# Performance work log

Measured on AMD Instinct MI355X. Metric: run time of the kernel, lower is better.

Reference implementation:

```python
import jax, jax.numpy as jnp
import numpy as np
from jax import lax

B, C, H, W = 2, 96, 96, 96
N = 8            # d_state
R = C // 16      # dt_rank = 6
K = 4            # scan directions


def _gn(x, g, b, eps=1e-5):
    # GroupNorm(num_groups=1): normalize over (C,H,W) per sample, per-channel affine
    mu = jnp.mean(x, axis=(1, 2, 3), keepdims=True)
    var = jnp.var(x, axis=(1, 2, 3), keepdims=True)
    xn = (x - mu) * jax.lax.rsqrt(var + eps)
    return xn * g[None, :, None, None] + b[None, :, None, None]


def _conv1x1(x, w, b):
    return jnp.einsum('bchw,oc->bohw', x, w) + b[None, :, None, None]


def _ss2d(x, xproj_w, dt_w, dt_b, A_log, Ds):
    # x: [B,C,H,W]. 4-directional selective scan (VMamba SS2D core).
    Bn, Cc, Hh, Ww = x.shape
    L = Hh * Ww
    x_hw = x.reshape(Bn, Cc, L)                                   # row-major
    x_wh = jnp.transpose(x, (0, 1, 3, 2)).reshape(Bn, Cc, L)      # col-major
    xs = jnp.stack([x_hw, x_wh, x_hw[..., ::-1], x_wh[..., ::-1]], axis=1)  # [B,K,C,L]
    xdbl = jnp.einsum('bkcl,kdc->bkdl', xs, xproj_w)              # [B,K,R+2N,L]
    dts, Bs, Cs = jnp.split(xdbl, [R, R + N], axis=2)             # [B,K,R,L],[B,K,N,L],[B,K,N,L]
    dts = jax.nn.softplus(jnp.einsum('bkrl,kcr->bkcl', dts, dt_w) + dt_b[None, :, :, None])  # [B,K,C,L]
    A = -jnp.exp(A_log)                                           # [K,C,N]
    dA = jnp.exp(dts[:, :, :, None, :] * A[None, :, :, :, None])                    # [B,K,C,N,L]
    dBx = dts[:, :, :, None, :] * Bs[:, :, None, :, :] * xs[:, :, :, None, :]       # [B,K,C,N,L]

    def comb(e1, e2):
        a1, b1 = e1
        a2, b2 = e2
        return a1 * a2, a2 * b1 + b2

    _, hs = lax.associative_scan(comb, (dA, dBx), axis=-1)        # h_t = dA_t*h_{t-1} + dBx_t
    ys = jnp.einsum('bkcnl,bknl->bkcl', hs, Cs) + Ds[None, :, :, None] * xs
    y0 = ys[:, 0]
    y1 = jnp.transpose(ys[:, 1].reshape(Bn, Cc, Ww, Hh), (0, 1, 3, 2)).reshape(Bn, Cc, L)
    y2 = ys[:, 2][..., ::-1]
    y3 = jnp.transpose(ys[:, 3][..., ::-1].reshape(Bn, Cc, Ww, Hh), (0, 1, 3, 2)).reshape(Bn, Cc, L)
    return (y0 + y1 + y2 + y3).reshape(Bn, Cc, Hh, Ww)


def setup_inputs() -> dict:
    key = jax.random.key(0)
    ks = jax.random.split(key, 12)
    f = lambda k, sh: jax.random.normal(k, sh, jnp.float32) * 0.02
    return {
        'x': jax.random.normal(ks[0], (B, C, H, W), jnp.float32),
        'ln_g': jnp.ones((C,), jnp.float32), 'ln_b': jnp.zeros((C,), jnp.float32),
        'p1_w': f(ks[1], (C, C)), 'p1_b': jnp.zeros((C,), jnp.float32),
        'p2_w': f(ks[2], (C, C)), 'p2_b': jnp.zeros((C,), jnp.float32),
        'dw_w': f(ks[3], (C, 1, 3, 3)), 'dw_b': jnp.zeros((C,), jnp.float32),
        'xproj_w': f(ks[4], (K, R + 2 * N, C)),
        'dt_w': f(ks[5], (K, C, R)), 'dt_b': f(ks[6], (K, C)),
        'A_log': jnp.log(jnp.broadcast_to(jnp.arange(1, N + 1, dtype=jnp.float32), (K, C, N))),
        'Ds': jnp.ones((K, C), jnp.float32),
        'n2_g': jnp.ones((C,), jnp.float32), 'n2_b': jnp.zeros((C,), jnp.float32),
        'ca_w1': f(ks[7], (C // 8, C)), 'ca_b1': jnp.zeros((C // 8,), jnp.float32),
        'ca_w2': f(ks[8], (C, C // 8)), 'ca_b2': jnp.zeros((C,), jnp.float32),
    }


def reference(x, ln_g, ln_b, p1_w, p1_b, p2_w, p2_b, dw_w, dw_b,
              xproj_w, dt_w, dt_b, A_log, Ds, n2_g, n2_b,
              ca_w1, ca_b1, ca_w2, ca_b2):
    h = _gn(x, ln_g, ln_b)
    a = jax.nn.silu(_conv1x1(h, p1_w, p1_b))                       # path 1
    b = _conv1x1(h, p2_w, p2_b)                                    # path 2
    b = lax.conv_general_dilated(b, dw_w, (1, 1), ((1, 1), (1, 1)),
                                 feature_group_count=C,
                                 dimension_numbers=('NCHW', 'OIHW', 'NCHW'))
    b = b + dw_b[None, :, None, None]
    b = jax.nn.silu(b)
    b = _ss2d(b, xproj_w, dt_w, dt_b, A_log, Ds)
    b = _gn(b, n2_g, n2_b)
    y = a * b
    # channel attention (SE-style, reduction 8)
    s = jnp.mean(y, axis=(2, 3))                                   # [B,C]
    z = jax.nn.relu(s @ ca_w1.T + ca_b1)
    attn = jax.nn.sigmoid(z @ ca_w2.T + ca_b2)
    y = y * attn[:, :, None, None]
    return x + y
```

## Files before the change

### kernel.cpp

```cpp
#include <hip/hip_runtime.h>
#include <hip/hip_bf16.h>
#include <cmath>
#include <cstdint>

constexpr int B_ = 2, C_ = 96, H_ = 96, W_ = 96, L_ = H_ * W_;
constexpr int N_ = 8, R_ = 6, K_ = 4, D_ = R_ + 2 * N_;
constexpr int CH_ = 128, G_ = L_ / CH_;
constexpr int JS_ = 4, SEG_ = CH_ / JS_;
constexpr int S_ = G_ * JS_;
constexpr float EPS_ = 1e-5f;

__device__ __forceinline__ float silu_f(float v) { return v / (1.f + __expf(-v)); }
__device__ __forceinline__ float softplus_f(float t) {
    return fmaxf(t, 0.f) + __logf(1.f + __expf(-fabsf(t)));
}

__device__ __forceinline__ void block_reduce2(float& a, float& b) {
    #pragma unroll
    for (int o = 32; o; o >>= 1) { a += __shfl_xor(a, o); b += __shfl_xor(b, o); }
    __shared__ float la[4], lb[4];
    int wid = threadIdx.x >> 6;
    if ((threadIdx.x & 63) == 0) { la[wid] = a; lb[wid] = b; }
    __syncthreads();
    if (threadIdx.x == 0) { a = la[0] + la[1] + la[2] + la[3]; b = lb[0] + lb[1] + lb[2] + lb[3]; }
}

__global__ __launch_bounds__(256) void stats_kernel(const float* __restrict__ in,
                                                    float* __restrict__ stats, int outbase) {
    int b = blockIdx.y;
    const float* p = in + (size_t)b * ((size_t)C_ * L_);
    float s = 0.f, s2 = 0.f;
    const int total = C_ * L_;
    for (int i = blockIdx.x * 256 + threadIdx.x; i < total; i += gridDim.x * 256) {
        float v = p[i];
        s += v;
        s2 = fmaf(v, v, s2);
    }
    block_reduce2(s, s2);
    if (threadIdx.x == 0) {
        atomicAdd(&stats[outbase + 2 * b], s);
        atomicAdd(&stats[outbase + 2 * b + 1], s2);
    }
}

__global__ __launch_bounds__(256) void conv1x1_kernel(
    const float* __restrict__ x, const float* __restrict__ stats,
    const float* __restrict__ lng, const float* __restrict__ lnb,
    const float* __restrict__ w1, const float* __restrict__ b1,
    const float* __restrict__ w2, const float* __restrict__ b2,
    float* __restrict__ a, float* __restrict__ bpre) {
    constexpr int OG = 8;
    int b = blockIdx.z;
    int o0 = blockIdx.y * OG;
    int l = blockIdx.x * 256 + threadIdx.x;

    constexpr float inv = 1.f / (float)(C_ * L_);
    float mu = stats[2 * b] * inv;
    float var = stats[2 * b + 1] * inv - mu * mu;
    float rs = rsqrtf(var + EPS_);

    __shared__ float sw1[OG][C_], sw2[OG][C_], sg[C_], so[C_];
    for (int i = threadIdx.x; i < OG * C_; i += 256) {
        int j = i / C_, c = i % C_;
        sw1[j][c] = w1[(o0 + j) * C_ + c];
        sw2[j][c] = w2[(o0 + j) * C_ + c];
    }
    for (int i = threadIdx.x; i < C_; i += 256) {
        float g = lng[i];
        sg[i] = g * rs;
        so[i] = lnb[i] - mu * rs * g;
    }
    __syncthreads();

    const float* xb = x + (size_t)b * C_ * L_ + l;
    float acc1[OG], acc2[OG];
    #pragma unroll
    for (int j = 0; j < OG; ++j) { acc1[j] = b1[o0 + j]; acc2[j] = b2[o0 + j]; }
    for (int c = 0; c < C_; ++c) {
        float hv = fmaf(xb[(size_t)c * L_], sg[c], so[c]);
        #pragma unroll
        for (int j = 0; j < OG; ++j) {
            acc1[j] = fmaf(hv, sw1[j][c], acc1[j]);
            acc2[j] = fmaf(hv, sw2[j][c], acc2[j]);
        }
    }
    #pragma unroll
    for (int j = 0; j < OG; ++j) {
        size_t o = ((size_t)(b * C_ + o0 + j)) * L_ + l;
        a[o] = silu_f(acc1[j]);
        bpre[o] = acc2[j];
    }
}

__global__ __launch_bounds__(256) void dw_kernel(const float* __restrict__ bp,
                                                 const float* __restrict__ wgt,
                                                 const float* __restrict__ bias,
                                                 float* __restrict__ u) {
    int b = blockIdx.z, c = blockIdx.y;
    int pix = blockIdx.x * 256 + threadIdx.x;
    int h = pix / W_, w = pix % W_;
    const float* in = bp + ((size_t)(b * C_ + c)) * L_;
    const float* kw = wgt + c * 9;
    float acc = bias[c];
    #pragma unroll
    for (int dh = -1; dh <= 1; ++dh) {
        int hh = h + dh;
        if (hh < 0 || hh >= H_) continue;
        #pragma unroll
        for (int dw = -1; dw <= 1; ++dw) {
            int ww = w + dw;
            if (ww < 0 || ww >= W_) continue;
            acc = fmaf(in[hh * W_ + ww], kw[(dh + 1) * 3 + (dw + 1)], acc);
        }
    }
    u[((size_t)(b * C_ + c)) * L_ + pix] = silu_f(acc);
}

__global__ __launch_bounds__(256) void transpose_kernel(const float* __restrict__ u,
                                                        float* __restrict__ u_t) {
    int w0 = blockIdx.x * 32;
    int c = blockIdx.y, b = blockIdx.z;
    __shared__ float ts[96][33];
    const float* src = u + ((size_t)(b * C_ + c)) * L_;
    float* dst = u_t + ((size_t)(b * C_ + c)) * L_;
    for (int idx = threadIdx.x; idx < 96 * 32; idx += 256) {
        int hh = idx >> 5, ww = idx & 31;
        ts[hh][ww] = src[hh * 96 + w0 + ww];
    }
    __syncthreads();
    for (int idx = threadIdx.x; idx < 32 * 96; idx += 256) {
        int ww = idx / 96, hh = idx % 96;
        dst[(w0 + ww) * 96 + hh] = ts[hh][ww];
    }
}

__global__ __launch_bounds__(256) void proj_kernel(
    const float* __restrict__ u, const float* __restrict__ u_t,
    const float* __restrict__ xproj,
    float* __restrict__ dts, float* __restrict__ Bsb, float* __restrict__ Csb) {
    int b = blockIdx.z, k = blockIdx.y;
    int pos = threadIdx.x & 63, cg = threadIdx.x >> 6;
    int l = blockIdx.x * 64 + pos;

    __shared__ float sxp[C_][24];
    __shared__ float red[D_][4][64];
    for (int i = threadIdx.x; i < D_ * C_; i += 256) {
        int d = i / C_, c = i % C_;
        sxp[c][d] = xproj[(k * D_ + d) * C_ + c];
    }
    __syncthreads();

    const float* src = ((k & 1) ? u_t : u) + (size_t)b * C_ * L_;
    int posIdx = (k < 2) ? l : (L_ - 1 - l);
    const float* sp = src + (size_t)(cg * 24) * L_ + posIdx;

    float acc[D_];
    #pragma unroll
    for (int d = 0; d < D_; ++d) acc[d] = 0.f;
    #pragma unroll 4
    for (int ci = 0; ci < 24; ++ci) {
        int c = cg * 24 + ci;
        float xv = sp[(size_t)ci * L_];
        float w[22];
        *(float4*)&w[0]  = *(const float4*)&sxp[c][0];
        *(float4*)&w[4]  = *(const float4*)&sxp[c][4];
        *(float4*)&w[8]  = *(const float4*)&sxp[c][8];
        *(float4*)&w[12] = *(const float4*)&sxp[c][12];
        *(float4*)&w[16] = *(const float4*)&sxp[c][16];
        *(float2*)&w[20] = *(const float2*)&sxp[c][20];
        #pragma unroll
        for (int d = 0; d < D_; ++d) acc[d] = fmaf(xv, w[d], acc[d]);
    }
    #pragma unroll
    for (int d = 0; d < D_; ++d) red[d][cg][pos] = acc[d];
    __syncthreads();

    if (cg == 0) {
        #pragma unroll
        for (int r = 0; r < R_; ++r) {
            float s = red[r][0][pos] + red[r][1][pos] + red[r][2][pos] + red[r][3][pos];
            dts[((size_t)((b * K_ + k) * R_ + r)) * L_ + l] = s;
        }
    } else if (cg == 1) {
        #pragma unroll
        for (int n = 0; n < N_; ++n) {
            int d = R_ + n;
            float s = red[d][0][pos] + red[d][1][pos] + red[d][2][pos] + red[d][3][pos];
            Bsb[((size_t)((b * K_ + k) * N_ + n)) * L_ + l] = s;
        }
    } else if (cg == 2) {
        #pragma unroll
        for (int n = 0; n < N_; ++n) {
            int d = R_ + N_ + n;
            float s = red[d][0][pos] + red[d][1][pos] + red[d][2][pos] + red[d][3][pos];
            Csb[((size_t)((b * K_ + k) * N_ + n)) * L_ + l] = s;
        }
    }
}


__global__ __launch_bounds__(192) void scan1_kernel(
    const float* __restrict__ dts, const float* __restrict__ dtw,
    const float* __restrict__ dtbv, const float* __restrict__ Bs,
    const float* __restrict__ u, const float* __restrict__ u_t,
    const float* __restrict__ A_log,
    float* __restrict__ carA, float* __restrict__ carB) {
    int g = blockIdx.x >> 1, chalf = blockIdx.x & 1;
    int k = blockIdx.y, b = blockIdx.z;
    int c0 = chalf * 48;
    const int t = threadIdx.x;
    const int l0 = g * CH_;

    __shared__ float u_s[48][132];
    __shared__ float B_s[128][12];
    __shared__ float T_s[128][8];

    const float* usrc = ((k & 1) ? u_t : u) + (size_t)b * C_ * L_ + (size_t)c0 * L_;
    if (k < 2) {
        for (int idx = t; idx < 48 * 32; idx += 192) {
            int c2 = idx >> 5, q = idx & 31;
            *(float4*)&u_s[c2][q * 4] = *(const float4*)(usrc + (size_t)c2 * L_ + l0 + q * 4);
        }
    } else {
        for (int idx = t; idx < 48 * 32; idx += 192) {
            int c2 = idx >> 5, q = idx & 31;
            float4 v = *(const float4*)(usrc + (size_t)c2 * L_ + (L_ - l0 - q * 4 - 4));
            u_s[c2][q * 4 + 0] = v.w; u_s[c2][q * 4 + 1] = v.z;
            u_s[c2][q * 4 + 2] = v.y; u_s[c2][q * 4 + 3] = v.x;
        }
    }
    const float* Bg = Bs + ((size_t)(b * K_ + k)) * N_ * L_ + l0;
    for (int idx = t; idx < 8 * 32; idx += 192) {
        int n = idx >> 5, q = idx & 31;
        float4 v = *(const float4*)(Bg + (size_t)n * L_ + q * 4);
        B_s[q * 4 + 0][n] = v.x; B_s[q * 4 + 1][n] = v.y;
        B_s[q * 4 + 2][n] = v.z; B_s[q * 4 + 3][n] = v.w;
    }
    const float* Tg = dts + ((size_t)(b * K_ + k)) * R_ * L_ + l0;
    for (int idx = t; idx < 6 * 32; idx += 192) {
        int r = idx >> 5, q = idx & 31;
        float4 v = *(const float4*)(Tg + (size_t)r * L_ + q * 4);
        T_s[q * 4 + 0][r] = v.x; T_s[q * 4 + 1][r] = v.y;
        T_s[q * 4 + 2][r] = v.z; T_s[q * 4 + 3][r] = v.w;
    }
    __syncthreads();

    int cc = t % 48, j = t / 48;
    int c = c0 + cc;
    float A[N_];
    #pragma unroll
    for (int n = 0; n < N_; ++n) A[n] = -__expf(A_log[(k * C_ + c) * N_ + n]);
    float wdt[R_];
    #pragma unroll
    for (int r = 0; r < R_; ++r) wdt[r] = dtw[(k * C_ + c) * R_ + r];
    float bdt = dtbv[k * C_ + c];

    float ap[N_], h[N_];
    #pragma unroll
    for (int n = 0; n < N_; ++n) { ap[n] = 1.f; h[n] = 0.f; }
    int i0 = j * SEG_;
    for (int ii = 0; ii < SEG_; ii += 4) {
        float4 x4 = *(float4*)&u_s[cc][i0 + ii];
        float xx[4] = {x4.x, x4.y, x4.z, x4.w};
        #pragma unroll
        for (int s = 0; s < 4; ++s) {
            int i = i0 + ii + s;
            float4 t4 = *(float4*)&T_s[i][0];
            float2 t2 = *(float2*)&T_s[i][4];
            float tt = bdt;
            tt = fmaf(t4.x, wdt[0], tt); tt = fmaf(t4.y, wdt[1], tt);
            tt = fmaf(t4.z, wdt[2], tt); tt = fmaf(t4.w, wdt[3], tt);
            tt = fmaf(t2.x, wdt[4], tt); tt = fmaf(t2.y, wdt[5], tt);
            float d = softplus_f(tt);
            float dx = d * xx[s];
            float4 ba = *(float4*)&B_s[i][0];
            float4 bb = *(float4*)&B_s[i][4];
            float bv[8] = {ba.x, ba.y, ba.z, ba.w, bb.x, bb.y, bb.z, bb.w};
            #pragma unroll
            for (int n = 0; n < N_; ++n) {
                float da = __expf(d * A[n]);
                ap[n] *= da;
                h[n] = fmaf(da, h[n], bv[n] * dx);
            }
        }
    }
    size_t sidx = (((size_t)((b * K_ + k) * C_ + c)) * S_ + (g * JS_ + j)) * N_;
    #pragma unroll
    for (int n = 0; n < N_; ++n) { carA[sidx + n] = ap[n]; carB[sidx + n] = h[n]; }
}

__global__ __launch_bounds__(256) void scan2_kernel(const float* __restrict__ carA,
                                                    const float* __restrict__ carB,
                                                    float* __restrict__ hinit) {
    int tid = blockIdx.x * 256 + threadIdx.x;
    if (tid >= B_ * K_ * C_ * N_) return;
    int n = tid & 7;
    size_t rowb = (size_t)(tid >> 3) * S_;
    float h = 0.f;
    for (int s = 0; s < S_; s += 8) {
        float av[8], bv[8];
        #pragma unroll
        for (int q = 0; q < 8; ++q) {
            size_t idx = (rowb + s + q) * N_ + n;
            av[q] = carA[idx]; bv[q] = carB[idx];
        }
        #pragma unroll
        for (int q = 0; q < 8; ++q) {
            size_t idx = (rowb + s + q) * N_ + n;
            hinit[idx] = h;
            h = fmaf(av[q], h, bv[q]);
        }
    }
}

__global__ __launch_bounds__(192) void scan3_kernel(
    const float* __restrict__ dts, const float* __restrict__ dtw,
    const float* __restrict__ dtbv, const float* __restrict__ Bs,
    const float* __restrict__ Cs, const float* __restrict__ u,
    const float* __restrict__ u_t, const float* __restrict__ A_log,
    const float* __restrict__ Dsv, const float* __restrict__ hinit,
    float* __restrict__ ydir) {
    int g = blockIdx.x >> 1, chalf = blockIdx.x & 1;
    int k = blockIdx.y, b = blockIdx.z;
    int c0 = chalf * 48;
    const int t = threadIdx.x;
    const int l0 = g * CH_;

    __shared__ float u_s[48][132];
    __shared__ float B_s[128][12];
    __shared__ float C_s[128][12];
    __shared__ float T_s[128][8];

    const float* usrc = ((k & 1) ? u_t : u) + (size_t)b * C_ * L_ + (size_t)c0 * L_;
    if (k < 2) {
        for (int idx = t; idx < 48 * 32; idx += 192) {
            int c2 = idx >> 5, q = idx & 31;
            *(float4*)&u_s[c2][q * 4] = *(const float4*)(usrc + (size_t)c2 * L_ + l0 + q * 4);
        }
    } else {
        for (int idx = t; idx < 48 * 32; idx += 192) {
            int c2 = idx >> 5, q = idx & 31;
            float4 v = *(const float4*)(usrc + (size_t)c2 * L_ + (L_ - l0 - q * 4 - 4));
            u_s[c2][q * 4 + 0] = v.w; u_s[c2][q * 4 + 1] = v.z;
            u_s[c2][q * 4 + 2] = v.y; u_s[c2][q * 4 + 3] = v.x;
        }
    }
    const float* Bg = Bs + ((size_t)(b * K_ + k)) * N_ * L_ + l0;
    const float* Cg = Cs + ((size_t)(b * K_ + k)) * N_ * L_ + l0;
    for (int idx = t; idx < 8 * 32; idx += 192) {
        int n = idx >> 5, q = idx & 31;
        float4 v = *(const float4*)(Bg + (size_t)n * L_ + q * 4);
        B_s[q * 4 + 0][n] = v.x; B_s[q * 4 + 1][n] = v.y;
        B_s[q * 4 + 2][n] = v.z; B_s[q * 4 + 3][n] = v.w;
        float4 w = *(const float4*)(Cg + (size_t)n * L_ + q * 4);
        C_s[q * 4 + 0][n] = w.x; C_s[q * 4 + 1][n] = w.y;
        C_s[q * 4 + 2][n] = w.z; C_s[q * 4 + 3][n] = w.w;
    }
    const float* Tg = dts + ((size_t)(b * K_ + k)) * R_ * L_ + l0;
    for (int idx = t; idx < 6 * 32; idx += 192) {
        int r = idx >> 5, q = idx & 31;
        float4 v = *(const float4*)(Tg + (size_t)r * L_ + q * 4);
        T_s[q * 4 + 0][r] = v.x; T_s[q * 4 + 1][r] = v.y;
        T_s[q * 4 + 2][r] = v.z; T_s[q * 4 + 3][r] = v.w;
    }
    __syncthreads();

    int cc = t % 48, j = t / 48;
    int c = c0 + cc;
    float A[N_];
    #pragma unroll
    for (int n = 0; n < N_; ++n) A[n] = -__expf(A_log[(k * C_ + c) * N_ + n]);
    float wdt[R_];
    #pragma unroll
    for (int r = 0; r < R_; ++r) wdt[r] = dtw[(k * C_ + c) * R_ + r];
    float bdt = dtbv[k * C_ + c];
    float Dv = Dsv[k * C_ + c];

    float h[N_];
    size_t sidx = (((size_t)((b * K_ + k) * C_ + c)) * S_ + (g * JS_ + j)) * N_;
    #pragma unroll
    for (int n = 0; n < N_; ++n) h[n] = hinit[sidx + n];

    int i0 = j * SEG_;
    for (int ii = 0; ii < SEG_; ii += 4) {
        float4 x4 = *(float4*)&u_s[cc][i0 + ii];
        float xx[4] = {x4.x, x4.y, x4.z, x4.w};
        #pragma unroll
        for (int s = 0; s < 4; ++s) {
            int i = i0 + ii + s;
            float4 t4 = *(float4*)&T_s[i][0];
            float2 t2 = *(float2*)&T_s[i][4];
            float tt = bdt;
            tt = fmaf(t4.x, wdt[0], tt); tt = fmaf(t4.y, wdt[1], tt);
            tt = fmaf(t4.z, wdt[2], tt); tt = fmaf(t4.w, wdt[3], tt);
            tt = fmaf(t2.x, wdt[4], tt); tt = fmaf(t2.y, wdt[5], tt);
            float d = softplus_f(tt);
            float dx = d * xx[s];
            float4 ba = *(float4*)&B_s[i][0];
            float4 bb = *(float4*)&B_s[i][4];
            float4 ca = *(float4*)&C_s[i][0];
            float4 cb = *(float4*)&C_s[i][4];
            float bv[8] = {ba.x, ba.y, ba.z, ba.w, bb.x, bb.y, bb.z, bb.w};
            float cv[8] = {ca.x, ca.y, ca.z, ca.w, cb.x, cb.y, cb.z, cb.w};
            float y = Dv * xx[s];
            #pragma unroll
            for (int n = 0; n < N_; ++n) {
                float da = __expf(d * A[n]);
                h[n] = fmaf(da, h[n], bv[n] * dx);
                y = fmaf(cv[n], h[n], y);
            }
            u_s[cc][i] = y;
        }
    }
    __syncthreads();
    float* yg = ydir + ((size_t)((b * K_ + k) * C_ + c0)) * L_ + l0;
    for (int idx = t; idx < 48 * 32; idx += 192) {
        int c2 = idx >> 5, q = idx & 31;
        *(float4*)(yg + (size_t)c2 * L_ + q * 4) = *(float4*)&u_s[c2][q * 4];
    }
}

__global__ __launch_bounds__(256) void merge_kernel(const float* __restrict__ ydir,
                                                    float* __restrict__ ysum,
                                                    float* __restrict__ stats) {
    int h0 = blockIdx.x * 32;
    int c = blockIdx.y, b = blockIdx.z;
    __shared__ float t1[96][33], t3[96][33];
    const float* y0p = ydir + ((size_t)((b * K_ + 0) * C_ + c)) * L_;
    const float* y1p = ydir + ((size_t)((b * K_ + 1) * C_ + c)) * L_;
    const float* y2p = ydir + ((size_t)((b * K_ + 2) * C_ + c)) * L_;
    const float* y3p = ydir + ((size_t)((b * K_ + 3) * C_ + c)) * L_;
    for (int idx = threadIdx.x; idx < 96 * 32; idx += 256) {
        int w = idx >> 5, hh = idx & 31;
        t1[w][hh] = y1p[w * 96 + h0 + hh];
        t3[w][hh] = y3p[L_ - 1 - (w * 96 + h0 + hh)];
    }
    __syncthreads();
    float s = 0.f, s2 = 0.f;
    float* yout = ysum + ((size_t)(b * C_ + c)) * L_;
    for (int idx = threadIdx.x; idx < 32 * 96; idx += 256) {
        int hh = idx / 96, w = idx % 96;
        int pix = (h0 + hh) * 96 + w;
        float v = y0p[pix] + y2p[L_ - 1 - pix] + t1[w][hh] + t3[w][hh];
        yout[pix] = v;
        s += v;
        s2 = fmaf(v, v, s2);
    }
    block_reduce2(s, s2);
    if (threadIdx.x == 0) {
        atomicAdd(&stats[4 + 2 * b], s);
        atomicAdd(&stats[5 + 2 * b], s2);
    }
}

__global__ __launch_bounds__(256) void gn2_kernel(
    const float* __restrict__ ysum, const float* __restrict__ a,
    const float* __restrict__ stats, const float* __restrict__ g2,
    const float* __restrict__ b2, float* __restrict__ yv, float* __restrict__ svec) {
    int b = blockIdx.z, c = blockIdx.y;
    int pix = blockIdx.x * 256 + threadIdx.x;
    constexpr float inv = 1.f / (float)(C_ * L_);
    float mu = stats[4 + 2 * b] * inv;
    float var = stats[5 + 2 * b] * inv - mu * mu;
    float rs = rsqrtf(var + EPS_);
    size_t o = ((size_t)(b * C_ + c)) * L_ + pix;
    float bn = fmaf((ysum[o] - mu) * rs, g2[c], b2[c]);
    float y = a[o] * bn;
    yv[o] = y;

    float s = y;
    #pragma unroll
    for (int off = 32; off; off >>= 1) s += __shfl_xor(s, off);
    __shared__ float ls[4];
    if ((threadIdx.x & 63) == 0) ls[threadIdx.x >> 6] = s;
    __syncthreads();
    if (threadIdx.x == 0) atomicAdd(&svec[b * C_ + c], ls[0] + ls[1] + ls[2] + ls[3]);
}

__global__ __launch_bounds__(128) void attn_kernel(
    const float* __restrict__ svec, const float* __restrict__ w1,
    const float* __restrict__ b1, const float* __restrict__ w2,
    const float* __restrict__ b2, float* __restrict__ attn) {
    int b = blockIdx.x;
    __shared__ float ss[C_];
    __shared__ float zz[C_ / 8];
    int t = threadIdx.x;
    if (t < C_) ss[t] = svec[b * C_ + t] * (1.f / (float)L_);
    __syncthreads();
    if (t < C_ / 8) {
        float acc = b1[t];
        for (int c = 0; c < C_; ++c) acc = fmaf(w1[t * C_ + c], ss[c], acc);
        zz[t] = fmaxf(acc, 0.f);
    }
    __syncthreads();
    if (t < C_) {
        float acc = b2[t];
        #pragma unroll
        for (int j = 0; j < C_ / 8; ++j) acc = fmaf(w2[t * (C_ / 8) + j], zz[j], acc);
        attn[b * C_ + t] = 1.f / (1.f + __expf(-acc));
    }
}

__global__ __launch_bounds__(256) void final_kernel(const float* __restrict__ x,
                                                    const float* __restrict__ yv,
                                                    const float* __restrict__ attn,
                                                    float* __restrict__ out) {
    int b = blockIdx.z, c = blockIdx.y;
    int pix = blockIdx.x * 256 + threadIdx.x;
    size_t o = ((size_t)(b * C_ + c)) * L_ + pix;
    out[o] = fmaf(yv[o], attn[b * C_ + c], x[o]);
}

extern "C" void kernel_launch(void* const* d_in, const int* in_sizes, int n_in,
                              void* d_out, int out_size, void* d_ws, size_t ws_size,
                              hipStream_t stream) {
    const float* x    = (const float*)d_in[0];
    const float* ln_g = (const float*)d_in[1];
    const float* ln_b = (const float*)d_in[2];
    const float* p1w  = (const float*)d_in[3];
    const float* p1b  = (const float*)d_in[4];
    const float* p2w  = (const float*)d_in[5];
    const float* p2b  = (const float*)d_in[6];
    const float* dww  = (const float*)d_in[7];
    const float* dwb  = (const float*)d_in[8];
    const float* xprj = (const float*)d_in[9];
    const float* dtw  = (const float*)d_in[10];
    const float* dtb  = (const float*)d_in[11];
    const float* Alog = (const float*)d_in[12];
    const float* Dsp  = (const float*)d_in[13];
    const float* n2g  = (const float*)d_in[14];
    const float* n2b  = (const float*)d_in[15];
    const float* caw1 = (const float*)d_in[16];
    const float* cab1 = (const float*)d_in[17];
    const float* caw2 = (const float*)d_in[18];
    const float* cab2 = (const float*)d_in[19];
    float* out = (float*)d_out;

    const size_t BCL = (size_t)B_ * C_ * L_ * sizeof(float);
    char* ws = (char*)d_ws;
    size_t off = 0;
    float* stats = (float*)(ws + off); off += 4096;
    float* a     = (float*)(ws + off); off += BCL;
    float* bpre  = (float*)(ws + off); off += BCL;
    float* u     = (float*)(ws + off); off += BCL;
    float* u_t   = (float*)(ws + off); off += BCL;
    float* dts   = (float*)(ws + off); off += (size_t)B_ * K_ * R_ * L_ * sizeof(float);
    float* Bsb   = (float*)(ws + off); off += (size_t)B_ * K_ * N_ * L_ * sizeof(float);
    float* Csb   = (float*)(ws + off); off += (size_t)B_ * K_ * N_ * L_ * sizeof(float);
    float* carB  = (float*)(ws + off); off += (size_t)B_ * K_ * C_ * S_ * N_ * sizeof(float);
    float* hinit = (float*)(ws + off); off += (size_t)B_ * K_ * C_ * S_ * N_ * sizeof(float);
    float* ydir  = (float*)(ws + off); off += (size_t)B_ * K_ * C_ * L_ * sizeof(float);
    float* carA = bpre;
    float* ysum = u;
    float* yv   = ydir;

    hipMemsetAsync(stats, 0, 4096, stream);

    stats_kernel<<<dim3(432, 2), 256, 0, stream>>>(x, stats, 0);
    conv1x1_kernel<<<dim3(36, 12, 2), 256, 0, stream>>>(x, stats, ln_g, ln_b,
                                                        p1w, p1b, p2w, p2b, a, bpre);
    dw_kernel<<<dim3(36, 96, 2), 256, 0, stream>>>(bpre, dww, dwb, u);
    transpose_kernel<<<dim3(3, 96, 2), 256, 0, stream>>>(u, u_t);
    proj_kernel<<<dim3(144, 4, 2), 256, 0, stream>>>(u, u_t, xprj, dts, Bsb, Csb);
    scan1_kernel<<<dim3(2 * G_, K_, B_), 192, 0, stream>>>(dts, dtw, dtb, Bsb, u, u_t,
                                                           Alog, carA, carB);
    scan2_kernel<<<24, 256, 0, stream>>>(carA, carB, hinit);
    scan3_kernel<<<dim3(2 * G_, K_, B_), 192, 0, stream>>>(dts, dtw, dtb, Bsb, Csb, u, u_t,
                                                           Alog, Dsp, hinit, ydir);
    merge_kernel<<<dim3(3, 96, 2), 256, 0, stream>>>(ydir, ysum, stats);
    gn2_kernel<<<dim3(36, 96, 2), 256, 0, stream>>>(ysum, a, stats, n2g, n2b, yv, stats + 16);
    attn_kernel<<<2, 128, 0, stream>>>(stats + 16, caw1, cab1, caw2, cab2, stats + 256);
    final_kernel<<<dim3(36, 96, 2), 256, 0, stream>>>(x, yv, stats + 256, out);
}
```

Measured before the change: 331.4 us.

## Fold GN into conv weights, fuse dwconv+transpose, and fold GN2 into SE statistics

A prep kernel pre-scales the 1x1 conv weights by the GroupNorm gain and precomputes per-output bias terms, so the conv loop becomes a plain FMA with the normalization applied once per output. The depthwise conv and the transpose are merged into one shared-memory stripe kernel that writes u and u_t together. The merge kernel also accumulates per-channel sums of a and a*ysum, so the SE mean is derived algebraically and the gn2 pass and the yv buffer are no longer needed. This removes two full-tensor passes and one launch, at the cost of a serial single-block prep kernel and a formula for the channel mean that is more sensitive to rounding.

```diff
diff --git a/kernel.cpp b/kernel.cpp
--- a/kernel.cpp
+++ b/kernel.cpp
@@ -25,8 +25,26 @@
     if (threadIdx.x == 0) { a = la[0] + la[1] + la[2] + la[3]; b = lb[0] + lb[1] + lb[2] + lb[3]; }
 }
 
+__device__ __forceinline__ void block_reduce4(float& a, float& b, float& c, float& d) {
+    #pragma unroll
+    for (int o = 32; o; o >>= 1) {
+        a += __shfl_xor(a, o); b += __shfl_xor(b, o);
+        c += __shfl_xor(c, o); d += __shfl_xor(d, o);
+    }
+    __shared__ float ls[4][4];
+    int wid = threadIdx.x >> 6;
+    if ((threadIdx.x & 63) == 0) { ls[wid][0] = a; ls[wid][1] = b; ls[wid][2] = c; ls[wid][3] = d; }
+    __syncthreads();
+    if (threadIdx.x == 0) {
+        a = ls[0][0] + ls[1][0] + ls[2][0] + ls[3][0];
+        b = ls[0][1] + ls[1][1] + ls[2][1] + ls[3][1];
+        c = ls[0][2] + ls[1][2] + ls[2][2] + ls[3][2];
+        d = ls[0][3] + ls[1][3] + ls[2][3] + ls[3][3];
+    }
+}
+
 __global__ __launch_bounds__(256) void stats_kernel(const float* __restrict__ in,
-                                                    float* __restrict__ stats, int outbase) {
+                                                    float* __restrict__ stats) {
     int b = blockIdx.y;
     const float* p = in + (size_t)b * ((size_t)C_ * L_);
     float s = 0.f, s2 = 0.f;
@@ -38,20 +56,39 @@
     }
     block_reduce2(s, s2);
     if (threadIdx.x == 0) {
-        atomicAdd(&stats[outbase + 2 * b], s);
-        atomicAdd(&stats[outbase + 2 * b + 1], s2);
-    }
+        atomicAdd(&stats[2 * b], s);
+        atomicAdd(&stats[2 * b + 1], s2);
+    }
+}
+
+__global__ __launch_bounds__(192) void prep_kernel(
+    const float* __restrict__ lng, const float* __restrict__ lnb,
+    const float* __restrict__ w1, const float* __restrict__ w2,
+    float* __restrict__ wmt, float* __restrict__ pq) {
+    int t = threadIdx.x;
+    int mat = t / 96, o = t % 96;
+    const float* w = (mat == 0 ? w1 : w2) + o * C_;
+    float* dst = wmt + ((size_t)(mat * 12 + o / 8) * C_) * 8 + (o % 8);
+    float P = 0.f, Q = 0.f;
+    for (int c = 0; c < C_; ++c) {
+        float wv = w[c];
+        float g = lng[c];
+        P = fmaf(lnb[c], wv, P);
+        Q = fmaf(g, wv, Q);
+        dst[c * 8] = g * wv;
+    }
+    pq[mat * 192 + o] = P;
+    pq[mat * 192 + 96 + o] = Q;
 }
 
 __global__ __launch_bounds__(256) void conv1x1_kernel(
     const float* __restrict__ x, const float* __restrict__ stats,
-    const float* __restrict__ lng, const float* __restrict__ lnb,
-    const float* __restrict__ w1, const float* __restrict__ b1,
-    const float* __restrict__ w2, const float* __restrict__ b2,
+    const float* __restrict__ wmt, const float* __restrict__ pq,
+    const float* __restrict__ b1, const float* __restrict__ b2,
     float* __restrict__ a, float* __restrict__ bpre) {
     constexpr int OG = 8;
-    int b = blockIdx.z;
-    int o0 = blockIdx.y * OG;
+    int b = blockIdx.z, by = blockIdx.y;
+    int o0 = by * OG;
     int l = blockIdx.x * 256 + threadIdx.x;
 
     constexpr float inv = 1.f / (float)(C_ * L_);
@@ -59,78 +96,90 @@
     float var = stats[2 * b + 1] * inv - mu * mu;
     float rs = rsqrtf(var + EPS_);
 
-    __shared__ float sw1[OG][C_], sw2[OG][C_], sg[C_], so[C_];
-    for (int i = threadIdx.x; i < OG * C_; i += 256) {
-        int j = i / C_, c = i % C_;
-        sw1[j][c] = w1[(o0 + j) * C_ + c];
-        sw2[j][c] = w2[(o0 + j) * C_ + c];
-    }
-    for (int i = threadIdx.x; i < C_; i += 256) {
-        float g = lng[i];
-        sg[i] = g * rs;
-        so[i] = lnb[i] - mu * rs * g;
+    __shared__ float s1[C_][OG], s2[C_][OG];
+    const float* w1p = wmt + ((size_t)(0 * 12 + by) * C_) * 8;
+    const float* w2p = wmt + ((size_t)(1 * 12 + by) * C_) * 8;
+    for (int i = threadIdx.x; i < C_ * OG / 4; i += 256) {
+        ((float4*)s1)[i] = ((const float4*)w1p)[i];
+        ((float4*)s2)[i] = ((const float4*)w2p)[i];
     }
     __syncthreads();
 
     const float* xb = x + (size_t)b * C_ * L_ + l;
     float acc1[OG], acc2[OG];
     #pragma unroll
-    for (int j = 0; j < OG; ++j) { acc1[j] = b1[o0 + j]; acc2[j] = b2[o0 + j]; }
+    for (int j = 0; j < OG; ++j) { acc1[j] = 0.f; acc2[j] = 0.f; }
     for (int c = 0; c < C_; ++c) {
-        float hv = fmaf(xb[(size_t)c * L_], sg[c], so[c]);
-        #pragma unroll
-        for (int j = 0; j < OG; ++j) {
-            acc1[j] = fmaf(hv, sw1[j][c], acc1[j]);
-            acc2[j] = fmaf(hv, sw2[j][c], acc2[j]);
-        }
-    }
+        float xv = xb[(size_t)c * L_];
+        float4 wa = *(const float4*)&s1[c][0];
+        float4 wb = *(const float4*)&s1[c][4];
+        float4 wc = *(const float4*)&s2[c][0];
+        float4 wd = *(const float4*)&s2[c][4];
+        acc1[0] = fmaf(xv, wa.x, acc1[0]); acc1[1] = fmaf(xv, wa.y, acc1[1]);
+        acc1[2] = fmaf(xv, wa.z, acc1[2]); acc1[3] = fmaf(xv, wa.w, acc1[3]);
+        acc1[4] = fmaf(xv, wb.x, acc1[4]); acc1[5] = fmaf(xv, wb.y, acc1[5]);
+        acc1[6] = fmaf(xv, wb.z, acc1[6]); acc1[7] = fmaf(xv, wb.w, acc1[7]);
+        acc2[0] = fmaf(xv, wc.x, acc2[0]); acc2[1] = fmaf(xv, wc.y, acc2[1]);
+        acc2[2] = fmaf(xv, wc.z, acc2[2]); acc2[3] = fmaf(xv, wc.w, acc2[3]);
+        acc2[4] = fmaf(xv, wd.x, acc2[4]); acc2[5] = fmaf(xv, wd.y, acc2[5]);
+        acc2[6] = fmaf(xv, wd.z, acc2[6]); acc2[7] = fmaf(xv, wd.w, acc2[7]);
+    }
+    float murs = mu * rs;
     #pragma unroll
     for (int j = 0; j < OG; ++j) {
-        size_t o = ((size_t)(b * C_ + o0 + j)) * L_ + l;
-        a[o] = silu_f(acc1[j]);
-        bpre[o] = acc2[j];
-    }
-}
-
-__global__ __launch_bounds__(256) void dw_kernel(const float* __restrict__ bp,
-                                                 const float* __restrict__ wgt,
-                                                 const float* __restrict__ bias,
-                                                 float* __restrict__ u) {
-    int b = blockIdx.z, c = blockIdx.y;
-    int pix = blockIdx.x * 256 + threadIdx.x;
-    int h = pix / W_, w = pix % W_;
+        int o = o0 + j;
+        size_t oo = ((size_t)(b * C_ + o)) * L_ + l;
+        float be1 = b1[o] + pq[o] - murs * pq[96 + o];
+        float be2 = b2[o] + pq[192 + o] - murs * pq[288 + o];
+        a[oo] = silu_f(fmaf(rs, acc1[j], be1));
+        bpre[oo] = fmaf(rs, acc2[j], be2);
+    }
+}
+
+__global__ __launch_bounds__(256) void dwt_kernel(const float* __restrict__ bp,
+                                                  const float* __restrict__ wgt,
+                                                  const float* __restrict__ bias,
+                                                  float* __restrict__ u,
+                                                  float* __restrict__ u_t) {
+    int stripe = blockIdx.x, c = blockIdx.y, b = blockIdx.z;
+    int h0 = stripe * 48;
+    __shared__ float in_s[50][96];
+    __shared__ float out_s[48][97];
     const float* in = bp + ((size_t)(b * C_ + c)) * L_;
+    for (int idx = threadIdx.x; idx < 50 * 96; idx += 256) {
+        int r = idx / 96, w = idx % 96;
+        int hh = h0 - 1 + r;
+        in_s[r][w] = (hh >= 0 && hh < 96) ? in[hh * 96 + w] : 0.f;
+    }
+    __syncthreads();
     const float* kw = wgt + c * 9;
-    float acc = bias[c];
-    #pragma unroll
-    for (int dh = -1; dh <= 1; ++dh) {
-        int hh = h + dh;
-        if (hh < 0 || hh >= H_) continue;
-        #pragma unroll
-        for (int dw = -1; dw <= 1; ++dw) {
-            int ww = w + dw;
-            if (ww < 0 || ww >= W_) continue;
-            acc = fmaf(in[hh * W_ + ww], kw[(dh + 1) * 3 + (dw + 1)], acc);
-        }
-    }
-    u[((size_t)(b * C_ + c)) * L_ + pix] = silu_f(acc);
-}
-
-__global__ __launch_bounds__(256) void transpose_kernel(const float* __restrict__ u,
-                                                        float* __restrict__ u_t) {
-    int w0 = blockIdx.x * 32;
-    int c = blockIdx.y, b = blockIdx.z;
-    __shared__ float ts[96][33];
-    const float* src = u + ((size_t)(b * C_ + c)) * L_;
-    float* dst = u_t + ((size_t)(b * C_ + c)) * L_;
-    for (int idx = threadIdx.x; idx < 96 * 32; idx += 256) {
-        int hh = idx >> 5, ww = idx & 31;
-        ts[hh][ww] = src[hh * 96 + w0 + ww];
-    }
-    __syncthreads();
-    for (int idx = threadIdx.x; idx < 32 * 96; idx += 256) {
-        int ww = idx / 96, hh = idx % 96;
-        dst[(w0 + ww) * 96 + hh] = ts[hh][ww];
+    float k0 = kw[0], k1 = kw[1], k2 = kw[2], k3 = kw[3], k4 = kw[4],
+          k5 = kw[5], k6 = kw[6], k7 = kw[7], k8 = kw[8];
+    float bs = bias[c];
+    float* up = u + ((size_t)(b * C_ + c)) * L_;
+    for (int idx = threadIdx.x; idx < 48 * 96; idx += 256) {
+        int r = idx / 96, w = idx % 96;
+        int ri = r + 1;
+        bool wl = (w > 0), wr = (w < 95);
+        float acc = bs;
+        acc = fmaf(wl ? in_s[ri - 1][w - 1] : 0.f, k0, acc);
+        acc = fmaf(in_s[ri - 1][w], k1, acc);
+        acc = fmaf(wr ? in_s[ri - 1][w + 1] : 0.f, k2, acc);
+        acc = fmaf(wl ? in_s[ri][w - 1] : 0.f, k3, acc);
+        acc = fmaf(in_s[ri][w], k4, acc);
+        acc = fmaf(wr ? in_s[ri][w + 1] : 0.f, k5, acc);
+        acc = fmaf(wl ? in_s[ri + 1][w - 1] : 0.f, k6, acc);
+        acc = fmaf(in_s[ri + 1][w], k7, acc);
+        acc = fmaf(wr ? in_s[ri + 1][w + 1] : 0.f, k8, acc);
+        float v = silu_f(acc);
+        up[(h0 + r) * 96 + w] = v;
+        out_s[r][w] = v;
+    }
+    __syncthreads();
+    float* tp = u_t + ((size_t)(b * C_ + c)) * L_;
+    for (int idx = threadIdx.x; idx < 96 * 48; idx += 256) {
+        int w = idx / 48, r = idx % 48;
+        tp[w * 96 + h0 + r] = out_s[r][w];
     }
 }
 
@@ -421,6 +470,7 @@
 }
 
 __global__ __launch_bounds__(256) void merge_kernel(const float* __restrict__ ydir,
+                                                    const float* __restrict__ a,
                                                     float* __restrict__ ysum,
                                                     float* __restrict__ stats) {
     int h0 = blockIdx.x * 32;
@@ -436,79 +486,81 @@
         t3[w][hh] = y3p[L_ - 1 - (w * 96 + h0 + hh)];
     }
     __syncthreads();
-    float s = 0.f, s2 = 0.f;
+    float s = 0.f, s2 = 0.f, m0 = 0.f, m1 = 0.f;
     float* yout = ysum + ((size_t)(b * C_ + c)) * L_;
+    const float* ap = a + ((size_t)(b * C_ + c)) * L_;
     for (int idx = threadIdx.x; idx < 32 * 96; idx += 256) {
         int hh = idx / 96, w = idx % 96;
         int pix = (h0 + hh) * 96 + w;
         float v = y0p[pix] + y2p[L_ - 1 - pix] + t1[w][hh] + t3[w][hh];
+        float av = ap[pix];
         yout[pix] = v;
         s += v;
         s2 = fmaf(v, v, s2);
-    }
-    block_reduce2(s, s2);
+        m0 += av;
+        m1 = fmaf(av, v, m1);
+    }
+    block_reduce4(s, s2, m0, m1);
     if (threadIdx.x == 0) {
         atomicAdd(&stats[4 + 2 * b], s);
         atomicAdd(&stats[5 + 2 * b], s2);
-    }
-}
-
-__global__ __launch_bounds__(256) void gn2_kernel(
-    const float* __restrict__ ysum, const float* __restrict__ a,
+        atomicAdd(&stats[16 + b * C_ + c], m0);
+        atomicAdd(&stats[256 + b * C_ + c], m1);
+    }
+}
+
+__global__ __launch_bounds__(128) void attn_kernel(
     const float* __restrict__ stats, const float* __restrict__ g2,
-    const float* __restrict__ b2, float* __restrict__ yv, float* __restrict__ svec) {
+    const float* __restrict__ b2, const float* __restrict__ w1,
+    const float* __restrict__ b1, const float* __restrict__ w2,
+    const float* __restrict__ b2a, float* __restrict__ attn) {
+    int b = blockIdx.x;
+    constexpr float inv = 1.f / (float)(C_ * L_);
+    float mu = stats[4 + 2 * b] * inv;
+    float var = stats[5 + 2 * b] * inv - mu * mu;
+    float rs = rsqrtf(var + EPS_);
+    __shared__ float ss[C_];
+    __shared__ float zz[12];
+    int t = threadIdx.x;
+    if (t < C_) {
+        float M0 = stats[16 + b * C_ + t];
+        float M1 = stats[256 + b * C_ + t];
+        ss[t] = (g2[t] * rs * (M1 - mu * M0) + b2[t] * M0) * (1.f / (float)L_);
+    }
+    __syncthreads();
+    if (t < 12) {
+        float acc = b1[t];
+        for (int c = 0; c < C_; ++c) acc = fmaf(w1[t * C_ + c], ss[c], acc);
+        zz[t] = fmaxf(acc, 0.f);
+    }
+    __syncthreads();
+    if (t < C_) {
+        float acc = b2a[t];
+        #pragma unroll
+        for (int j = 0; j < 12; ++j) acc = fmaf(w2[t * 12 + j], zz[j], acc);
+        attn[b * C_ + t] = 1.f / (1.f + __expf(-acc));
+    }
+}
+
+__global__ __launch_bounds__(256) void final_kernel(const float* __restrict__ x,
+                                                    const float* __restrict__ ysum,
+                                                    const float* __restrict__ a,
+                                                    const float* __restrict__ stats,
+                                                    const float* __restrict__ g2,
+                                                    const float* __restrict__ b2,
+                                                    const float* __restrict__ attn,
+                                                    float* __restrict__ out) {
     int b = blockIdx.z, c = blockIdx.y;
     int pix = blockIdx.x * 256 + threadIdx.x;
     constexpr float inv = 1.f / (float)(C_ * L_);
     float mu = stats[4 + 2 * b] * inv;
     float var = stats[5 + 2 * b] * inv - mu * mu;
     float rs = rsqrtf(var + EPS_);
+    float gc = g2[c] * rs, bc = b2[c] - mu * rs * g2[c];
+    float at = attn[b * C_ + c];
     size_t o = ((size_t)(b * C_ + c)) * L_ + pix;
-    float bn = fmaf((ysum[o] - mu) * rs, g2[c], b2[c]);
-    float y = a[o] * bn;
-    yv[o] = y;
-
-    float s = y;
-    #pragma unroll
-    for (int off = 32; off; off >>= 1) s += __shfl_xor(s, off);
-    __shared__ float ls[4];
-    if ((threadIdx.x & 63) == 0) ls[threadIdx.x >> 6] = s;
-    __syncthreads();
-    if (threadIdx.x == 0) atomicAdd(&svec[b * C_ + c], ls[0] + ls[1] + ls[2] + ls[3]);
-}
-
-__global__ __launch_bounds__(128) void attn_kernel(
-    const float* __restrict__ svec, const float* __restrict__ w1,
-    const float* __restrict__ b1, const float* __restrict__ w2,
-    const float* __restrict__ b2, float* __restrict__ attn) {
-    int b = blockIdx.x;
-    __shared__ float ss[C_];
-    __shared__ float zz[C_ / 8];
-    int t = threadIdx.x;
-    if (t < C_) ss[t] = svec[b * C_ + t] * (1.f / (float)L_);
-    __syncthreads();
-    if (t < C_ / 8) {
-        float acc = b1[t];
-        for (int c = 0; c < C_; ++c) acc = fmaf(w1[t * C_ + c], ss[c], acc);
-        zz[t] = fmaxf(acc, 0.f);
-    }
-    __syncthreads();
-    if (t < C_) {
-        float acc = b2[t];
-        #pragma unroll
-        for (int j = 0; j < C_ / 8; ++j) acc = fmaf(w2[t * (C_ / 8) + j], zz[j], acc);
-        attn[b * C_ + t] = 1.f / (1.f + __expf(-acc));
-    }
-}
-
-__global__ __launch_bounds__(256) void final_kernel(const float* __restrict__ x,
-                                                    const float* __restrict__ yv,
-                                                    const float* __restrict__ attn,
-                                                    float* __restrict__ out) {
-    int b = blockIdx.z, c = blockIdx.y;
-    int pix = blockIdx.x * 256 + threadIdx.x;
-    size_t o = ((size_t)(b * C_ + c)) * L_ + pix;
-    out[o] = fmaf(yv[o], attn[b * C_ + c], x[o]);
+    float bn = fmaf(ysum[o], gc, bc);
+    out[o] = fmaf(a[o] * bn, at, x[o]);
 }
 
 extern "C" void kernel_launch(void* const* d_in, const int* in_sizes, int n_in,
@@ -540,6 +592,8 @@
     char* ws = (char*)d_ws;
     size_t off = 0;
     float* stats = (float*)(ws + off); off += 4096;
+    float* wmt   = (float*)(ws + off); off += 2 * 12 * 96 * 8 * sizeof(float);
+    float* pq    = (float*)(ws + off); off += 2 * 2 * 96 * sizeof(float);
     float* a     = (float*)(ws + off); off += BCL;
     float* bpre  = (float*)(ws + off); off += BCL;
     float* u     = (float*)(ws + off); off += BCL;
@@ -552,23 +606,21 @@
     float* ydir  = (float*)(ws + off); off += (size_t)B_ * K_ * C_ * L_ * sizeof(float);
     float* carA = bpre;
     float* ysum = u;
-    float* yv   = ydir;
+    float* attnv = stats + 512;
 
     hipMemsetAsync(stats, 0, 4096, stream);
 
-    stats_kernel<<<dim3(432, 2), 256, 0, stream>>>(x, stats, 0);
-    conv1x1_kernel<<<dim3(36, 12, 2), 256, 0, stream>>>(x, stats, ln_g, ln_b,
-                                                        p1w, p1b, p2w, p2b, a, bpre);
-    dw_kernel<<<dim3(36, 96, 2), 256, 0, stream>>>(bpre, dww, dwb, u);
-    transpose_kernel<<<dim3(3, 96, 2), 256, 0, stream>>>(u, u_t);
+    prep_kernel<<<1, 192, 0, stream>>>(ln_g, ln_b, p1w, p2w, wmt, pq);
+    stats_kernel<<<dim3(432, 2), 256, 0, stream>>>(x, stats);
+    conv1x1_kernel<<<dim3(36, 12, 2), 256, 0, stream>>>(x, stats, wmt, pq, p1b, p2b, a, bpre);
+    dwt_kernel<<<dim3(2, 96, 2), 256, 0, stream>>>(bpre, dww, dwb, u, u_t);
     proj_kernel<<<dim3(144, 4, 2), 256, 0, stream>>>(u, u_t, xprj, dts, Bsb, Csb);
     scan1_kernel<<<dim3(2 * G_, K_, B_), 192, 0, stream>>>(dts, dtw, dtb, Bsb, u, u_t,
                                                            Alog, carA, carB);
     scan2_kernel<<<24, 256, 0, stream>>>(carA, carB, hinit);
     scan3_kernel<<<dim3(2 * G_, K_, B_), 192, 0, stream>>>(dts, dtw, dtb, Bsb, Csb, u, u_t,
                                                            Alog, Dsp, hinit, ydir);
-    merge_kernel<<<dim3(3, 96, 2), 256, 0, stream>>>(ydir, ysum, stats);
-    gn2_kernel<<<dim3(36, 96, 2), 256, 0, stream>>>(ysum, a, stats, n2g, n2b, yv, stats + 16);
-    attn_kernel<<<2, 128, 0, stream>>>(stats + 16, caw1, cab1, caw2, cab2, stats + 256);
-    final_kernel<<<dim3(36, 96, 2), 256, 0, stream>>>(x, yv, stats + 256, out);
-}
+    merge_kernel<<<dim3(3, 96, 2), 256, 0, stream>>>(ydir, a, ysum, stats);
+    attn_kernel<<<2, 128, 0, stream>>>(stats, n2g, n2b, caw1, cab1, caw2, cab2, attnv);
+    final_kernel<<<dim3(36, 96, 2), 256, 0, stream>>>(x, ysum, a, stats, n2g, n2b, attnv, out);
+}
```

New measurement: 289.5 us. 12.7% less time.
